# Optimization experiments

Hardware: AMD Instinct MI355X
Metric: run time of the kernel (lower is better)

Reference implementation:

```python
import jax, jax.numpy as jnp
import numpy as np
from jax.scipy.special import erf, erfinv

SQRT2 = 1.4142135623730951
COST_CLASS, COST_BBOX, COST_GIOU = 1.0, 1.0, 1.0
NORM_MU, NORM_SIGMA = -5.5, 2.5        # torch.distributions.Normal(-5.5, 2.5)
HALFNORM_SCALE = 0.3                   # torch.distributions.HalfNormal(0.3)
LOOKAHEAD = 2


def box_cxcywh_to_xyxy(b):
    cx, cy, w, h = jnp.split(b, 4, axis=-1)
    return jnp.concatenate([cx - 0.5 * w, cy - 0.5 * h, cx + 0.5 * w, cy + 0.5 * h], axis=-1)


def generalized_box_iou(boxes1, boxes2):
    # boxes1 [M,4], boxes2 [N,4] in xyxy -> [M,N]
    area1 = (boxes1[:, 2] - boxes1[:, 0]) * (boxes1[:, 3] - boxes1[:, 1])
    area2 = (boxes2[:, 2] - boxes2[:, 0]) * (boxes2[:, 3] - boxes2[:, 1])
    lt = jnp.maximum(boxes1[:, None, :2], boxes2[None, :, :2])
    rb = jnp.minimum(boxes1[:, None, 2:], boxes2[None, :, 2:])
    wh = jnp.clip(rb - lt, 0.0)
    inter = wh[..., 0] * wh[..., 1]
    union = area1[:, None] + area2[None, :] - inter
    iou = inter / union
    lt2 = jnp.minimum(boxes1[:, None, :2], boxes2[None, :, :2])
    rb2 = jnp.maximum(boxes1[:, None, 2:], boxes2[None, :, 2:])
    wh2 = jnp.clip(rb2 - lt2, 0.0)
    area = wh2[..., 0] * wh2[..., 1]
    return iou - (area - union) / area


def build_fx_T(pred_logits, pred_boxes, tgt_boxes, tgt_labels, T):
    bs, Q, _ = pred_logits.shape
    N = tgt_labels.shape[0]  # bs * T
    out_prob = jax.nn.softmax(pred_logits.reshape(bs * Q, -1), axis=-1)
    out_bbox = pred_boxes.reshape(bs * Q, 4)
    cost_class = -out_prob[:, tgt_labels]                                       # [bs*Q, N]
    cost_bbox = jnp.sum(jnp.abs(out_bbox[:, None, :] - tgt_boxes[None, :, :]), axis=-1)  # L1 cdist
    cost_giou = -generalized_box_iou(box_cxcywh_to_xyxy(out_bbox), box_cxcywh_to_xyxy(tgt_boxes))
    C = COST_BBOX * cost_bbox + COST_CLASS * cost_class + COST_GIOU * cost_giou
    C = C.reshape(bs, Q, N)
    # permute(0,2,1) then block-diag boolean select: keep only same-batch target rows
    Cp = jnp.transpose(C, (0, 2, 1)).reshape(bs, bs, T, Q)
    Csel = Cp[jnp.arange(bs), jnp.arange(bs)].reshape(N, Q)                     # [N, Q]
    # prob = Normal(mu, sigma).cdf(-C); fx = HalfNormal(scale).icdf(prob)  (elementwise)
    prob = 0.5 * (1.0 + erf((-Csel - NORM_MU) / (NORM_SIGMA * SQRT2)))
    fx = HALFNORM_SCALE * SQRT2 * erfinv(prob)
    return fx.T                                                                 # [Q, N]


def batch_my_linear_sum_assignment(B, row_lookups):
    # B: [Q, N] float cost, row_lookups: [N, N] int block-diagonal 0/1 matrix.
    N = row_lookups.shape[-1]

    def step(B, _):
        # topk(clamp(B, max=100), 2, dim=0).values -> diff along dim 0 -> second_best - best
        top2 = jax.lax.top_k(jnp.minimum(B, 100.0).T, LOOKAHEAD)[0]   # [N, 2]
        delta = top2[:, 1] - top2[:, 0]                               # torch.diff(values, n=1, dim=0)
        col = jnp.argmax(jnp.abs(delta))
        row = jnp.argmax(B[:, col])
        B = B.at[:, col].set(0.0)
        # torch: B[row, row_lookups[col]] = 0  -- long 0/1 values used as COLUMN INDICES (faithful)
        B = B.at[row, row_lookups[col]].set(0.0)
        B = B.at[row, col].set(-1e-07)
        return B, None

    B, _ = jax.lax.scan(step, B, None, length=N)
    return B < 0


def setup_inputs() -> dict:
    key = jax.random.key(0)
    k1, k2, k3, k4 = jax.random.split(key, 4)
    bs, Q, num_classes, T = 32, 512, 92, 24
    N = bs * T
    return {
        "pred_logits": jax.random.normal(k1, (bs, Q, num_classes), dtype=jnp.float32),
        "pred_boxes": jax.random.uniform(k2, (bs, Q, 4), dtype=jnp.float32),
        "tgt_boxes": jax.random.uniform(k3, (N, 4), dtype=jnp.float32),
        "tgt_labels": jax.random.randint(k4, (N,), 0, num_classes),
        "num_targets_per_image": T,
    }


def reference(pred_logits, pred_boxes, tgt_boxes, tgt_labels, num_targets_per_image):
    bs = pred_logits.shape[0]
    T = int(num_targets_per_image)
    N = bs * T
    fx_T = build_fx_T(pred_logits, pred_boxes, tgt_boxes, tgt_labels, T)        # [Q, N]
    # lookup_sizes_vfast with uniform sizes: block-diagonal ones matrix [N, N]
    row_lookups = jnp.kron(jnp.eye(bs, dtype=jnp.int32), jnp.ones((T, T), dtype=jnp.int32))
    return batch_my_linear_sum_assignment(fx_T, row_lookups)                    # bool [Q, N]
```

## Files before the change

### kernel.cpp

```cpp
#include <hip/hip_runtime.h>
#include <math.h>

#pragma clang fp contract(off)

#define QN   512
#define NN   768
#define BSZ  32
#define TPI  24
#define NCLS 92

#define WFENCE() asm volatile("s_waitcnt lgkmcnt(0)" ::: "memory")


__device__ __forceinline__ float xla_erf_f32(float x) {
#pragma clang fp contract(off)
  float x2 = x * x;
  float p = -2.72614225801306e-10f;
  p = fmaf(x2, p, 2.77068142495902e-08f);
  p = fmaf(x2, p, -2.10102402082508e-06f);
  p = fmaf(x2, p, -5.69250639462346e-05f);
  p = fmaf(x2, p, -7.34990630326855e-04f);
  p = fmaf(x2, p, -2.95459980854025e-03f);
  p = fmaf(x2, p, -1.60960333262415e-02f);
  p = x * p;
  float q = -1.45660718464996e-05f;
  q = fmaf(x2, q, -2.13374055278905e-04f);
  q = fmaf(x2, q, -1.68282697438203e-03f);
  q = fmaf(x2, q, -7.37332916720468e-03f);
  q = fmaf(x2, q, -1.42647390514189e-02f);
  float r = p / q;
  if (fabsf(x) >= 3.832506856900711f) r = copysignf(1.0f, x);
  return r;
}

__device__ __forceinline__ float xla_erfinv_f32(float b) {
#pragma clang fp contract(off)
  float bb = b * b;
  float u = (-bb) + 1.0f;
  float w = -((float)log((double)u));
  float p;
  if (w < 5.0f) {
    float ww = w - 2.5f;
    p = 2.81022636e-08f;
    p = p * ww + 3.43273939e-07f;
    p = p * ww - 3.5233877e-06f;
    p = p * ww - 4.39150654e-06f;
    p = p * ww + 0.00021858087f;
    p = p * ww - 0.00125372503f;
    p = p * ww - 0.00417768164f;
    p = p * ww + 0.246640727f;
    p = p * ww + 1.50140941f;
  } else {
    float ww = (float)sqrt((double)w) - 3.0f;
    p = -0.000200214257f;
    p = p * ww + 0.000100950558f;
    p = p * ww + 0.00134934322f;
    p = p * ww - 0.00367342844f;
    p = p * ww + 0.00573950773f;
    p = p * ww - 0.0076224613f;
    p = p * ww + 0.00943887047f;
    p = p * ww + 1.00167406f;
    p = p * ww + 2.83297682f;
  }
  return p * b;
}


#define SROWS 64

__global__ void __launch_bounds__(256) k_softmax_stats(const float* __restrict__ logits,
                                                       float* __restrict__ mx,
                                                       float* __restrict__ sm) {
#pragma clang fp contract(off)
  __shared__ float buf[SROWS][NCLS + 1];
  int r0 = blockIdx.x * SROWS;
  const float* src = logits + (size_t)r0 * NCLS;
  for (int i = threadIdx.x; i < SROWS * NCLS; i += 256) {
    int rr = i / NCLS, cc = i - rr * NCLS;
    buf[rr][cc] = src[i];
  }
  __syncthreads();
  int r = threadIdx.x;
  if (r < SROWS) {
    const float* row = buf[r];
    float m = -INFINITY;
    for (int j = 0; j < NCLS; ++j) m = fmaxf(m, row[j]);
    float s = 0.0f;
    for (int j = 0; j < NCLS; ++j) s += expf(row[j] - m);
    mx[r0 + r] = m;
    sm[r0 + r] = s;
  }
}


__global__ void k_build(const float* __restrict__ logits,
                        const float* __restrict__ pboxes,
                        const float* __restrict__ tboxes,
                        const int* __restrict__ tlabels,
                        const float* __restrict__ mx,
                        const float* __restrict__ sm,
                        float* __restrict__ B) {
#pragma clang fp contract(off)
  int t = blockIdx.x * blockDim.x + threadIdx.x;
  if (t >= QN * NN) return;
  int n = t >> 9;
  int q = t & (QN - 1);
  int b = n / TPI;
  int r = b * QN + q;

  int lab = tlabels[n];
  float pc = expf(logits[(size_t)r * NCLS + lab] - mx[r]) / sm[r];
  float cost_class = -pc;

  float4 pb = ((const float4*)pboxes)[r];
  float4 tb = ((const float4*)tboxes)[n];

  float cost_bbox = ((fabsf(pb.x - tb.x) + fabsf(pb.y - tb.y)) +
                     fabsf(pb.z - tb.z)) + fabsf(pb.w - tb.w);

  float p0 = pb.x - 0.5f * pb.z;
  float p1 = pb.y - 0.5f * pb.w;
  float p2 = pb.x + 0.5f * pb.z;
  float p3 = pb.y + 0.5f * pb.w;
  float t0 = tb.x - 0.5f * tb.z;
  float t1 = tb.y - 0.5f * tb.w;
  float t2 = tb.x + 0.5f * tb.z;
  float t3 = tb.y + 0.5f * tb.w;

  float area1 = (p2 - p0) * (p3 - p1);
  float area2 = (t2 - t0) * (t3 - t1);
  float ltx = fmaxf(p0, t0), lty = fmaxf(p1, t1);
  float rbx = fminf(p2, t2), rby = fminf(p3, t3);
  float whx = fmaxf(rbx - ltx, 0.0f), why = fmaxf(rby - lty, 0.0f);
  float inter = whx * why;
  float uni = (area1 + area2) - inter;
  float iou = inter / uni;
  float l2x = fminf(p0, t0), l2y = fminf(p1, t1);
  float r2x = fmaxf(p2, t2), r2y = fmaxf(p3, t3);
  float w2x = fmaxf(r2x - l2x, 0.0f), w2y = fmaxf(r2y - l2y, 0.0f);
  float area = w2x * w2y;
  float giou = iou - (area - uni) / area;

  float C = (cost_bbox + cost_class) + (-giou);

  float z = (-C + 5.5f) / 3.5355339059327378f;
  float prob = 0.5f * (1.0f + xla_erf_f32(z));
  float fx = 0.4242640687119285f * xla_erfinv_f32(prob);

  B[t] = fx;
}


__global__ void k_init(const float* __restrict__ B, float* __restrict__ ad,
                       int* __restrict__ am) {
  int n = blockIdx.x * 4 + (threadIdx.x >> 6);
  int lane = threadIdx.x & 63;
  const float* cp = B + (size_t)n * QN;
  float v1 = -INFINITY, v2 = -INFINITY, bv = -INFINITY;
  int bi = QN;
#pragma unroll
  for (int k = 0; k < QN / 64; ++k) {
    float raw = cp[lane + 64 * k];
    float v = fminf(raw, 100.0f);
    if (v > v1) { v2 = v1; v1 = v; }
    else if (v > v2) v2 = v;
    if (raw > bv) { bv = raw; bi = lane + 64 * k; }
  }
  for (int off = 32; off > 0; off >>= 1) {
    float o1 = __shfl_xor(v1, off), o2 = __shfl_xor(v2, off);
    float ov = __shfl_xor(bv, off); int oi = __shfl_xor(bi, off);
    if (o1 > v1) { v2 = fmaxf(v1, o2); v1 = o1; }
    else v2 = fmaxf(v2, o1);
    if (ov > bv || (ov == bv && oi < bi)) { bv = ov; bi = oi; }
  }
  if (lane == 0) { ad[n] = v1 - v2; am[n] = bi; }
}


__device__ __forceinline__ void wave_maxcount(const float* arr, int lane, float bound,
                                              float& mx, int& cnt) {
  float m = -INFINITY; int c = 0;
#pragma unroll
  for (int k = 0; k < QN / 64; ++k) {
    float v = fminf(arr[lane + 64 * k], 100.0f);
    if (v < bound) {
      if (v > m) { m = v; c = 1; }
      else if (v == m) c++;
    }
  }
  for (int off = 32; off > 0; off >>= 1) {
    float om = __shfl_xor(m, off);
    int oc = __shfl_xor(c, off);
    if (om > m) { m = om; c = oc; }
    else if (om == m) c += oc;
  }
  mx = m; cnt = c;
}

__device__ __forceinline__ int wave_argmax(const float* arr, int lane) {
  float bv = -INFINITY; int bi = 0x7fffffff;
#pragma unroll
  for (int k = 0; k < QN / 64; ++k) {
    float v = arr[lane + 64 * k];
    if (v > bv) { bv = v; bi = lane + 64 * k; }
  }
  for (int off = 32; off > 0; off >>= 1) {
    float ov = __shfl_xor(bv, off);
    int oi = __shfl_xor(bi, off);
    if (ov > bv || (ov == bv && oi < bi)) { bv = ov; bi = oi; }
  }
  return bi;
}

__device__ __forceinline__ bool ms_update(float x, float& a1, int& c1, float& a2, int& c2) {
  x = fminf(x, 100.0f);
  bool rescan = false;
  if (x == a1) {
    if (--c1 == 0) rescan = true;
  } else if (x == a2) {
    if (--c2 == 0) rescan = true;
  }
  if (!rescan) {
    if (0.0f > a1) { a2 = a1; c2 = c1; a1 = 0.0f; c1 = 1; }
    else if (0.0f == a1) c1++;
    else if (0.0f > a2) { a2 = 0.0f; c2 = 1; }
    else if (0.0f == a2) c2++;
  }
  return rescan;
}


__global__ void __launch_bounds__(256) k_scan(const float* __restrict__ B,
                                              const float* __restrict__ ad_g,
                                              const int* __restrict__ am_g,
                                              int* __restrict__ asg_out) {
  __shared__ unsigned long long skey[1024];
  __shared__ unsigned long long spay[1024];
  __shared__ float m0[QN];
  __shared__ float m1[QN];
  __shared__ int   asg[NN];
  __shared__ int   minpos[QN];
  __shared__ float fst[4];
  __shared__ int   ist[4];
  const int tid  = threadIdx.x;
  const int lane = tid & 63;
  const int wave = tid >> 6;

  for (int i = tid; i < QN; i += 256) {
    m0[i] = B[i];
    m1[i] = B[QN + i];
    minpos[i] = 0x7fffffff;
  }
  for (int i = tid; i < NN; i += 256) {
    asg[i] = -1;
    unsigned long long key = 0ull;
    if (i >= 2) {
      unsigned vb = __float_as_uint(ad_g[i]);
      unsigned lo = ((unsigned)(1023 - i) << 16) | (unsigned)am_g[i];
      key = ((unsigned long long)vb << 32) | (unsigned long long)lo;
    }
    skey[i] = key;
  }
  for (int i = NN + tid; i < 1024; i += 256) skey[i] = 0ull;
  __syncthreads();

  for (int kk2 = 2; kk2 <= 1024; kk2 <<= 1) {
    for (int j = kk2 >> 1; j > 0; j >>= 1) {
#pragma unroll
      for (int k = 0; k < 2; ++k) {
        int g = tid + 256 * k;
        int t = ((g & ~(j - 1)) << 1) | (g & (j - 1));
        int l = t | j;
        unsigned long long a = skey[t], b = skey[l];
        bool sw = ((t & kk2) == 0) ? (a < b) : (a > b);
        if (sw) { skey[t] = b; skey[l] = a; }
      }
      __syncthreads();
    }
  }

#pragma unroll
  for (int k = 0; k < 4; ++k) {
    int pp = tid + 256 * k;
    unsigned long long key = skey[pp];
    int r = (int)(key & 0x1FF);
    spay[pp] = (unsigned long long)__float_as_uint(fminf(m0[r], 100.0f)) |
               ((unsigned long long)__float_as_uint(fminf(m1[r], 100.0f)) << 32);
    if (key != 0ull) atomicMin(&minpos[r], pp);
  }
  __syncthreads();
#pragma unroll
  for (int k = 0; k < 4; ++k) {
    int pp = tid + 256 * k;
    unsigned long long key = skey[pp];
    int r = (int)(key & 0x1FF);
    if (key != 0ull && minpos[r] == pp) skey[pp] |= 0x8000ull;
  }
  if (wave == 0) {
    float A1, A2; int C1, C2;
    wave_maxcount(m0, lane, INFINITY, A1, C1);
    wave_maxcount(m0, lane, A1, A2, C2);
    if (lane == 0) { fst[0] = A1; fst[1] = A2; ist[0] = C1; ist[1] = C2; }
  } else if (wave == 1) {
    float B1, B2; int D1, D2;
    wave_maxcount(m1, lane, INFINITY, B1, D1);
    wave_maxcount(m1, lane, B1, B2, D2);
    if (lane == 0) { fst[2] = B1; fst[3] = B2; ist[2] = D1; ist[3] = D2; }
  }
  __syncthreads();
  if (wave != 0) return;

  float a1 = fst[0], a2 = fst[1], b1 = fst[2], b2 = fst[3];
  int   c1 = ist[0], c2 = ist[1], d1 = ist[2], d2 = ist[3];

  int p = 0, it = 0, w0 = -64;
  float cv = 0.0f, ix0 = 0.0f, ix1 = 0.0f;
  unsigned lo = 0; int row = 0; bool ft = false;
  int negpos0 = -1, negpos1 = -1, dt_m0 = -1, dt_m1 = -1;
  bool trivial0 = false, trivial1 = false;
  int asg0 = -1, asg1 = -1;

  while (it < NN) {
    if (p >= w0 + 64) {
      w0 = p & ~63;
      unsigned long long kk = skey[w0 + lane];
      unsigned long long yy = spay[w0 + lane];
      cv  = __uint_as_float((unsigned)(kk >> 32));
      lo  = (unsigned)kk;
      row = (int)(lo & 0x1FF);
      ft  = (lo & 0x8000u) != 0;
      ix0 = __uint_as_float((unsigned)yy);
      ix1 = __uint_as_float((unsigned)(yy >> 32));
    }
    float gap0 = (c1 >= 2) ? 0.0f : (a1 - a2);
    float gap1 = (d1 >= 2) ? 0.0f : (b1 - b2);
    float best = fmaxf(gap0, gap1);

    float x0 = trivial0 ? ((row == negpos0) ? -1e-07f : 0.0f)
                        : ((ft && row != dt_m0) ? ix0 : 0.0f);
    float x1 = trivial1 ? ((row == negpos1) ? -1e-07f : 0.0f)
                        : ((ft && row != dt_m1) ? ix1 : 0.0f);
    bool slow = ((!trivial0) && !(a1 > 0.0f && a2 > 0.0f)) ||
                ((!trivial1) && !(b1 > 0.0f && b2 > 0.0f));
    bool ev = slow ||
              (trivial0 ? (x0 != 0.0f) : (x0 == a1 || x0 == a2)) ||
              (trivial1 ? (x1 != 0.0f) : (x1 == b1 || x1 == b2));
    bool sel = !(cv > best);

    int base = p - w0;
    unsigned long long valid = ~0ull << base;
    unsigned long long selm = __ballot(sel) & valid;
    unsigned long long evm  = __ballot(ev)  & valid;
    int lsel = selm ? (int)__builtin_ctzll(selm) : 64;
    int lev  = evm  ? (int)__builtin_ctzll(evm)  : 64;
    int lmin = (lsel < lev) ? lsel : lev;
    int pref = lmin - base;
    int rem = NN - it;
    if (pref > rem) pref = rem;

    if ((int)lane >= base && (int)lane < base + pref) {
      m0[row] = 0.0f;
      m1[row] = 0.0f;
      asg[1023 - (int)(lo >> 16)] = row;
    }
    p += pref; it += pref;
    if (it >= NN) break;
    if (lmin == 64) continue;

    WFENCE();
    if (lsel <= lev) {
      int col = (gap1 > gap0) ? 1 : 0;
      if (col == 0) {
        int rw = trivial0 ? ((negpos0 == 0) ? 1 : 0) : wave_argmax(m0, lane);
        float x1p = m1[rw];
#pragma unroll
        for (int k = 0; k < QN / 64; ++k) m0[lane + 64 * k] = 0.0f;
        if (lane == 0) { m0[rw] = -1e-07f; m1[rw] = 0.0f; }
        WFENCE();
        a1 = 0.0f; c1 = QN - 1; a2 = -1e-07f; c2 = 1;
        trivial0 = true; negpos0 = rw;
        dt_m1 = rw;
        if (negpos1 == rw) negpos1 = -1;
        if (ms_update(x1p, b1, d1, b2, d2)) {
          WFENCE();
          wave_maxcount(m1, lane, INFINITY, b1, d1);
          wave_maxcount(m1, lane, b1, b2, d2);
        }
        asg0 = rw;
        if (asg1 == rw) asg1 = -1;
      } else {
        int rw = trivial1 ? ((negpos1 == 0) ? 1 : 0) : wave_argmax(m1, lane);
        float x0p = m0[rw];
#pragma unroll
        for (int k = 0; k < QN / 64; ++k) m1[lane + 64 * k] = 0.0f;
        if (lane == 0) { m1[rw] = -1e-07f; m0[rw] = 0.0f; }
        WFENCE();
        b1 = 0.0f; d1 = QN - 1; b2 = -1e-07f; d2 = 1;
        trivial1 = true; negpos1 = rw;
        dt_m0 = rw;
        if (negpos0 == rw) negpos0 = -1;
        if (ms_update(x0p, a1, c1, a2, c2)) {
          WFENCE();
          wave_maxcount(m0, lane, INFINITY, a1, c1);
          wave_maxcount(m0, lane, a1, a2, c2);
        }
        asg1 = rw;
        if (asg0 == rw) asg0 = -1;
      }
      ++it;
    } else {
      float cx0 = __shfl(x0, lmin);
      float cx1 = __shfl(x1, lmin);
      int crow  = __shfl(row, lmin);
      int ccol  = 1023 - __shfl((int)(lo >> 16), lmin);
      if (lane == 0) { m0[crow] = 0.0f; m1[crow] = 0.0f; asg[ccol] = crow; }
      if (negpos0 == crow) negpos0 = -1;
      if (negpos1 == crow) negpos1 = -1;
      if (ms_update(cx0, a1, c1, a2, c2)) {
        WFENCE();
        wave_maxcount(m0, lane, INFINITY, a1, c1);
        wave_maxcount(m0, lane, a1, a2, c2);
      }
      if (ms_update(cx1, b1, d1, b2, d2)) {
        WFENCE();
        wave_maxcount(m1, lane, INFINITY, b1, d1);
        wave_maxcount(m1, lane, b1, b2, d2);
      }
      if (asg0 == crow) asg0 = -1;
      if (asg1 == crow) asg1 = -1;
      ++p; ++it;
    }
  }

  if (lane == 0) { asg[0] = asg0; asg[1] = asg1; }
  WFENCE();
#pragma unroll
  for (int k = 0; k < NN / 64; ++k) {
    int i = lane + 64 * k;
    asg_out[i] = asg[i];
  }
}


__global__ void k_out(const int* __restrict__ asg, int* __restrict__ out, int total) {
  int t = blockIdx.x * blockDim.x + threadIdx.x;
  if (t >= total) return;
  int q = t / NN;
  int n = t - q * NN;
  out[t] = (asg[n] == q) ? 1 : 0;
}

extern "C" void kernel_launch(void* const* d_in, const int* in_sizes, int n_in,
                              void* d_out, int out_size, void* d_ws, size_t ws_size,
                              hipStream_t stream) {
  const float* logits  = (const float*)d_in[0];
  const float* pboxes  = (const float*)d_in[1];
  const float* tboxes  = (const float*)d_in[2];
  const int*   tlabels = (const int*)d_in[3];

  float* B    = (float*)d_ws;
  float* mx   = B + QN * NN;
  float* sm   = mx + BSZ * QN;
  float* ad   = sm + BSZ * QN;
  int*   am   = (int*)(ad + NN);
  int*   asgg = am + NN;
  int*   out  = (int*)d_out;

  hipLaunchKernelGGL(k_softmax_stats, dim3((BSZ * QN) / SROWS), dim3(256), 0, stream,
                     logits, mx, sm);
  hipLaunchKernelGGL(k_build, dim3((QN * NN) / 256), dim3(256), 0, stream,
                     logits, pboxes, tboxes, tlabels, mx, sm, B);
  hipLaunchKernelGGL(k_init, dim3(NN / 4), dim3(256), 0, stream, B, ad, am);
  hipLaunchKernelGGL(k_scan, dim3(1), dim3(256), 0, stream, B, ad, am, asgg);
  hipLaunchKernelGGL(k_out, dim3((QN * NN) / 256), dim3(256), 0, stream,
                     asgg, out, QN * NN);
}
```

Before: 56.07 us.

## Fuse softmax, cost build and key init into one per-target kernel

Merges the softmax-stats, cost-matrix build and per-column top-2/argmax init kernels into one kernel with one block per target. The full Q×N cost matrix is no longer written or read back; only the first two rows needed by the scan are stored. The scan's sort keys are also built in this kernel rather than inside the single-block scan. In exchange, each block recomputes the softmax max and sum for all 512 query rows of its image, so those exp calls repeat 24 times per image. This also removes two kernel launches.

```diff
diff --git a/kernel.cpp b/kernel.cpp
--- a/kernel.cpp
+++ b/kernel.cpp
@@ -66,54 +66,12 @@
 }
 
 
-#define SROWS 64
-
-__global__ void __launch_bounds__(256) k_softmax_stats(const float* __restrict__ logits,
-                                                       float* __restrict__ mx,
-                                                       float* __restrict__ sm) {
+__device__ __forceinline__ float fx_rest(float pc, const float* __restrict__ pboxes,
+                                         float4 tb, int r) {
 #pragma clang fp contract(off)
-  __shared__ float buf[SROWS][NCLS + 1];
-  int r0 = blockIdx.x * SROWS;
-  const float* src = logits + (size_t)r0 * NCLS;
-  for (int i = threadIdx.x; i < SROWS * NCLS; i += 256) {
-    int rr = i / NCLS, cc = i - rr * NCLS;
-    buf[rr][cc] = src[i];
-  }
-  __syncthreads();
-  int r = threadIdx.x;
-  if (r < SROWS) {
-    const float* row = buf[r];
-    float m = -INFINITY;
-    for (int j = 0; j < NCLS; ++j) m = fmaxf(m, row[j]);
-    float s = 0.0f;
-    for (int j = 0; j < NCLS; ++j) s += expf(row[j] - m);
-    mx[r0 + r] = m;
-    sm[r0 + r] = s;
-  }
-}
-
-
-__global__ void k_build(const float* __restrict__ logits,
-                        const float* __restrict__ pboxes,
-                        const float* __restrict__ tboxes,
-                        const int* __restrict__ tlabels,
-                        const float* __restrict__ mx,
-                        const float* __restrict__ sm,
-                        float* __restrict__ B) {
-#pragma clang fp contract(off)
-  int t = blockIdx.x * blockDim.x + threadIdx.x;
-  if (t >= QN * NN) return;
-  int n = t >> 9;
-  int q = t & (QN - 1);
-  int b = n / TPI;
-  int r = b * QN + q;
-
-  int lab = tlabels[n];
-  float pc = expf(logits[(size_t)r * NCLS + lab] - mx[r]) / sm[r];
   float cost_class = -pc;
 
   float4 pb = ((const float4*)pboxes)[r];
-  float4 tb = ((const float4*)tboxes)[n];
 
   float cost_bbox = ((fabsf(pb.x - tb.x) + fabsf(pb.y - tb.y)) +
                      fabsf(pb.z - tb.z)) + fabsf(pb.w - tb.w);
@@ -145,27 +103,53 @@
 
   float z = (-C + 5.5f) / 3.5355339059327378f;
   float prob = 0.5f * (1.0f + xla_erf_f32(z));
-  float fx = 0.4242640687119285f * xla_erfinv_f32(prob);
-
-  B[t] = fx;
-}
-
-
-__global__ void k_init(const float* __restrict__ B, float* __restrict__ ad,
-                       int* __restrict__ am) {
-  int n = blockIdx.x * 4 + (threadIdx.x >> 6);
-  int lane = threadIdx.x & 63;
-  const float* cp = B + (size_t)n * QN;
-  float v1 = -INFINITY, v2 = -INFINITY, bv = -INFINITY;
-  int bi = QN;
-#pragma unroll
-  for (int k = 0; k < QN / 64; ++k) {
-    float raw = cp[lane + 64 * k];
-    float v = fminf(raw, 100.0f);
-    if (v > v1) { v2 = v1; v1 = v; }
-    else if (v > v2) v2 = v;
-    if (raw > bv) { bv = raw; bi = lane + 64 * k; }
-  }
+  return 0.4242640687119285f * xla_erfinv_f32(prob);
+}
+
+
+__global__ void __launch_bounds__(256) k_buildkey(const float* __restrict__ logits,
+                                                  const float* __restrict__ pboxes,
+                                                  const float* __restrict__ tboxes,
+                                                  const int* __restrict__ tlabels,
+                                                  float* __restrict__ B01,
+                                                  unsigned long long* __restrict__ skey_g) {
+#pragma clang fp contract(off)
+  __shared__ float w1s[4], w2s[4], wbs[4];
+  __shared__ int   wis[4];
+  const int n = blockIdx.x;
+  const int tid = threadIdx.x, lane = tid & 63, wave = tid >> 6;
+  const int lab = tlabels[n];
+  const float4 tb = ((const float4*)tboxes)[n];
+  const int rbase = (n / TPI) * QN;
+
+  float f[2];
+#pragma unroll
+  for (int k = 0; k < 2; ++k) {
+    int q = tid + 256 * k;
+    int r = rbase + q;
+    const float4* row4 = (const float4*)(logits + (size_t)r * NCLS);
+    float m = -INFINITY;
+#pragma unroll
+    for (int j = 0; j < NCLS / 4; ++j) {
+      float4 v = row4[j];
+      m = fmaxf(m, v.x); m = fmaxf(m, v.y); m = fmaxf(m, v.z); m = fmaxf(m, v.w);
+    }
+    float s = 0.0f;
+#pragma unroll
+    for (int j = 0; j < NCLS / 4; ++j) {
+      float4 v = row4[j];
+      s += expf(v.x - m); s += expf(v.y - m); s += expf(v.z - m); s += expf(v.w - m);
+    }
+    float gl = logits[(size_t)r * NCLS + lab];
+    float pc = expf(gl - m) / s;
+    f[k] = fx_rest(pc, pboxes, tb, r);
+    if (n < 2) B01[n * QN + q] = f[k];
+  }
+
+  float c0 = fminf(f[0], 100.0f), c1f = fminf(f[1], 100.0f);
+  float v1 = fmaxf(c0, c1f), v2 = fminf(c0, c1f);
+  float bv; int bi;
+  if (f[1] > f[0]) { bv = f[1]; bi = tid + 256; } else { bv = f[0]; bi = tid; }
   for (int off = 32; off > 0; off >>= 1) {
     float o1 = __shfl_xor(v1, off), o2 = __shfl_xor(v2, off);
     float ov = __shfl_xor(bv, off); int oi = __shfl_xor(bi, off);
@@ -173,12 +157,30 @@
     else v2 = fmaxf(v2, o1);
     if (ov > bv || (ov == bv && oi < bi)) { bv = ov; bi = oi; }
   }
-  if (lane == 0) { ad[n] = v1 - v2; am[n] = bi; }
+  if (lane == 0) { w1s[wave] = v1; w2s[wave] = v2; wbs[wave] = bv; wis[wave] = bi; }
+  __syncthreads();
+  if (tid == 0) {
+    float V1 = w1s[0], V2 = w2s[0], BV = wbs[0]; int BI = wis[0];
+    for (int w = 1; w < 4; ++w) {
+      float o1 = w1s[w], o2 = w2s[w];
+      if (o1 > V1) { V2 = fmaxf(V1, o2); V1 = o1; }
+      else V2 = fmaxf(V2, o1);
+      float ov = wbs[w]; int oi = wis[w];
+      if (ov > BV || (ov == BV && oi < BI)) { BV = ov; BI = oi; }
+    }
+    unsigned long long key = 0ull;
+    if (n >= 2) {
+      unsigned vb = __float_as_uint(V1 - V2);
+      key = ((unsigned long long)vb << 32) |
+            (unsigned long long)(((unsigned)(1023 - n) << 16) | (unsigned)BI);
+    }
+    skey_g[n] = key;
+  }
 }
 
 
 __device__ __forceinline__ void wave_maxcount(const float* arr, int lane, float bound,
-                                              float& mx, int& cnt) {
+                                              float& mxv, int& cnt) {
   float m = -INFINITY; int c = 0;
 #pragma unroll
   for (int k = 0; k < QN / 64; ++k) {
@@ -194,7 +196,7 @@
     if (om > m) { m = om; c = oc; }
     else if (om == m) c += oc;
   }
-  mx = m; cnt = c;
+  mxv = m; cnt = c;
 }
 
 __device__ __forceinline__ int wave_argmax(const float* arr, int lane) {
@@ -230,9 +232,8 @@
 }
 
 
-__global__ void __launch_bounds__(256) k_scan(const float* __restrict__ B,
-                                              const float* __restrict__ ad_g,
-                                              const int* __restrict__ am_g,
+__global__ void __launch_bounds__(256) k_scan(const float* __restrict__ B01,
+                                              const unsigned long long* __restrict__ skey_g,
                                               int* __restrict__ asg_out) {
   __shared__ unsigned long long skey[1024];
   __shared__ unsigned long long spay[1024];
@@ -247,20 +248,11 @@
   const int wave = tid >> 6;
 
   for (int i = tid; i < QN; i += 256) {
-    m0[i] = B[i];
-    m1[i] = B[QN + i];
+    m0[i] = B01[i];
+    m1[i] = B01[QN + i];
     minpos[i] = 0x7fffffff;
   }
-  for (int i = tid; i < NN; i += 256) {
-    asg[i] = -1;
-    unsigned long long key = 0ull;
-    if (i >= 2) {
-      unsigned vb = __float_as_uint(ad_g[i]);
-      unsigned lo = ((unsigned)(1023 - i) << 16) | (unsigned)am_g[i];
-      key = ((unsigned long long)vb << 32) | (unsigned long long)lo;
-    }
-    skey[i] = key;
-  }
+  for (int i = tid; i < NN; i += 256) { asg[i] = -1; skey[i] = skey_g[i]; }
   for (int i = NN + tid; i < 1024; i += 256) skey[i] = 0ull;
   __syncthreads();
 
@@ -458,20 +450,14 @@
   const float* tboxes  = (const float*)d_in[2];
   const int*   tlabels = (const int*)d_in[3];
 
-  float* B    = (float*)d_ws;
-  float* mx   = B + QN * NN;
-  float* sm   = mx + BSZ * QN;
-  float* ad   = sm + BSZ * QN;
-  int*   am   = (int*)(ad + NN);
-  int*   asgg = am + NN;
-  int*   out  = (int*)d_out;
-
-  hipLaunchKernelGGL(k_softmax_stats, dim3((BSZ * QN) / SROWS), dim3(256), 0, stream,
-                     logits, mx, sm);
-  hipLaunchKernelGGL(k_build, dim3((QN * NN) / 256), dim3(256), 0, stream,
-                     logits, pboxes, tboxes, tlabels, mx, sm, B);
-  hipLaunchKernelGGL(k_init, dim3(NN / 4), dim3(256), 0, stream, B, ad, am);
-  hipLaunchKernelGGL(k_scan, dim3(1), dim3(256), 0, stream, B, ad, am, asgg);
+  float* B01 = (float*)d_ws;
+  unsigned long long* skey_g = (unsigned long long*)(B01 + 1024);
+  int* asg_g = (int*)(skey_g + NN);
+  int* out = (int*)d_out;
+
+  hipLaunchKernelGGL(k_buildkey, dim3(NN), dim3(256), 0, stream,
+                     logits, pboxes, tboxes, tlabels, B01, skey_g);
+  hipLaunchKernelGGL(k_scan, dim3(1), dim3(256), 0, stream, B01, skey_g, asg_g);
   hipLaunchKernelGGL(k_out, dim3((QN * NN) / 256), dim3(256), 0, stream,
-                     asgg, out, QN * NN);
-}
+                     asg_g, out, QN * NN);
+}
```

Measured after the change: 63.60 us. +13.4%, slower.
